# Performance work log

Measured on AMD Instinct MI355X. Metric: run time of the kernel, lower is better.

Reference implementation:

```python
import jax, jax.numpy as jnp
import numpy as np

B, N, P, K, E = 4, 20000, 128, 128, 160000


def setup_inputs() -> dict:
    key = jax.random.key(0)
    ks = jax.random.split(key, 16)
    inv_p = 1.0 / np.sqrt(P)
    inv_3p = 1.0 / np.sqrt(3 * P)
    return {
        "x_in": jax.random.normal(ks[0], (B, N, P), jnp.float32),
        "vertex_areas": jax.random.uniform(ks[1], (B, N), jnp.float32, 1e-3, 1.0),
        "evals": jax.random.uniform(ks[2], (B, K), jnp.float32, 0.0, 10.0),
        "evecs": jax.random.normal(ks[3], (B, N, K), jnp.float32),
        "gradX_vals": jax.random.normal(ks[4], (B, E), jnp.float32),
        "gradY_vals": jax.random.normal(ks[5], (B, E), jnp.float32),
        "grad_rows": jax.random.randint(ks[6], (B, E), 0, N, jnp.int32),
        "grad_cols": jax.random.randint(ks[7], (B, E), 0, N, jnp.int32),
        # learned params
        "diffusion_times": jax.random.uniform(ks[8], (P,), jnp.float32, 1e-3, 0.1),
        "B_re": jax.random.normal(ks[9], (P, P), jnp.float32) * inv_p,
        "B_im": jax.random.normal(ks[10], (P, P), jnp.float32) * inv_p,
        "W1": jax.random.normal(ks[11], (P, 3 * P), jnp.float32) * inv_3p,
        "b1": jnp.zeros((P,), jnp.float32),
        "W2": jax.random.normal(ks[12], (P, P), jnp.float32) * inv_p,
        "b2": jnp.zeros((P,), jnp.float32),
        "W3": jax.random.normal(ks[13], (P, P), jnp.float32) * inv_p,
        "b3": jnp.zeros((P,), jnp.float32),
    }


def _spmm(rows, cols, vals, x):
    # sparse (n,n) @ dense (n,p) via COO gather/scatter
    return jax.ops.segment_sum(vals[:, None] * x[cols], rows, num_segments=x.shape[0])


def reference(x_in, vertex_areas, evals, evecs, gradX_vals, gradY_vals,
              grad_rows, grad_cols, diffusion_times, B_re, B_im,
              W1, b1, W2, b2, W3, b3):
    # SpectralDiffusion: project -> spectral heat scaling -> unproject
    times = jnp.clip(diffusion_times, 1e-8)                       # (P,)
    x_spec = jnp.einsum('bnk,bnp->bkp', evecs, x_in * vertex_areas[..., None])
    scale = jnp.exp(-evals[..., None] * times[None, None, :])     # (B,K,P)
    x_diffuse = jnp.einsum('bnk,bkp->bnp', evecs, scale * x_spec)  # (B,N,P)

    # sparse gradient halves
    gx = jax.vmap(_spmm)(grad_rows, grad_cols, gradX_vals, x_diffuse)  # (B,N,P)
    gy = jax.vmap(_spmm)(grad_rows, grad_cols, gradY_vals, x_diffuse)

    # SpatialGradient: tanh(re*B_re(re) + im*B_im(im))
    x_grad_features = jnp.tanh(gx * (gx @ B_re.T) + gy * (gy @ B_im.T))

    # MiniMLP on concatenated features (dropout inactive in eval)
    h = jnp.concatenate([x_in, x_diffuse, x_grad_features], axis=-1)  # (B,N,3P)
    h = jax.nn.relu(h @ W1.T + b1)
    h = jax.nn.relu(h @ W2.T + b2)
    h = h @ W3.T + b3
    return h + x_in
```

## Files before the change

kernel.cpp:

```cpp
#include <hip/hip_runtime.h>
#include <hip/hip_bf16.h>
#include <cstddef>

#define B_ 4
#define N_ 20000
#define P_ 128
#define K_ 128
#define E_ 160000

constexpr int NCH_S = 79;
constexpr int NSCB  = 79;

typedef __attribute__((ext_vector_type(8))) short short8;
typedef __attribute__((ext_vector_type(4))) float f32x4;

__device__ __forceinline__ unsigned pk2(float x, float y) {
  __hip_bfloat162 h = __float22bfloat162_rn(make_float2(x, y));
  union { __hip_bfloat162 h; unsigned u; } c; c.h = h; return c.u;
}
__device__ __forceinline__ float bf2f(short s) {
  union { unsigned u; float f; } c; c.u = ((unsigned)(unsigned short)s) << 16; return c.f;
}
__device__ __forceinline__ short f2bs(float x) {
  union { __hip_bfloat16 h; short s; } c; c.h = __float2bfloat16(x); return c.s;
}

__global__ __launch_bounds__(256)
void k_prep(const float* __restrict__ ev, const float* __restrict__ xin,
            const float* __restrict__ areas,
            __hip_bfloat16* __restrict__ evT, __hip_bfloat16* __restrict__ xT)
{
  const int tn = blockIdx.x, half = blockIdx.y & 1, mat = blockIdx.y >> 1;
  const int b = blockIdx.z, t = threadIdx.x;
  const int n0 = tn * 64, c0 = half * 64;
  __shared__ float ld[64][65];
  const float* src = (mat ? xin : ev) + (size_t)b * N_ * 128;
  const float* ab  = areas + (size_t)b * N_;
#pragma unroll
  for (int i = 0; i < 4; ++i) {
    int gid = t + i * 256;
    int r = gid >> 4, c4 = (gid & 15) << 2;
    int n = n0 + r;
    float4 v = make_float4(0.f, 0.f, 0.f, 0.f);
    if (n < N_) {
      v = *(const float4*)(src + (size_t)n * 128 + c0 + c4);
      if (mat == 0) { float ar = ab[n]; v.x *= ar; v.y *= ar; v.z *= ar; v.w *= ar; }
    }
    ld[r][c4] = v.x; ld[r][c4+1] = v.y; ld[r][c4+2] = v.z; ld[r][c4+3] = v.w;
  }
  __syncthreads();
  __hip_bfloat16* dst = (mat ? xT : evT) + (size_t)b * 128 * N_;
#pragma unroll
  for (int i = 0; i < 4; ++i) {
    int gid = t + i * 256;
    int cr = gid >> 4, nq = (gid & 15) << 2;
    int n = n0 + nq;
    if (n + 4 <= N_) {
      uint2 u;
      u.x = pk2(ld[nq][cr],   ld[nq+1][cr]);
      u.y = pk2(ld[nq+2][cr], ld[nq+3][cr]);
      *(uint2*)(dst + (size_t)(c0 + cr) * N_ + n) = u;
    }
  }
}

__global__ __launch_bounds__(256)
void k_wprep(const float* __restrict__ Bre, const float* __restrict__ Bim,
             uint4* __restrict__ WfRe, uint4* __restrict__ WfIm)
{
  int fid = blockIdx.x * 256 + threadIdx.x;
  if (fid >= 2048) return;
  int gg = fid >> 7, rr = fid & 127;
  const float* s0 = Bre + rr * 128 + gg * 8;
  const float* s1 = Bim + rr * 128 + gg * 8;
  float4 a0 = *(const float4*)s0, a1 = *(const float4*)(s0 + 4);
  uint4 u; u.x = pk2(a0.x, a0.y); u.y = pk2(a0.z, a0.w);
  u.z = pk2(a1.x, a1.y); u.w = pk2(a1.z, a1.w);
  WfRe[fid] = u;
  float4 b0 = *(const float4*)s1, b1 = *(const float4*)(s1 + 4);
  uint4 v; v.x = pk2(b0.x, b0.y); v.y = pk2(b0.z, b0.w);
  v.z = pk2(b1.x, b1.y); v.w = pk2(b1.z, b1.w);
  WfIm[fid] = v;
}

__global__ __launch_bounds__(256)
void k_wprep_mlp(const float* __restrict__ W1, const float* __restrict__ W2,
                 const float* __restrict__ W3, uint4* __restrict__ W1f,
                 uint4* __restrict__ W2f, uint4* __restrict__ W3f)
{
  int fid = blockIdx.x * 256 + threadIdx.x;
  if (fid >= 10240) return;
  int j = fid >> 11, wi = fid & 2047;
  int gg = wi >> 7, rr = wi & 127;
  const float* src;
  uint4* dst;
  if (j < 3)      { src = W1 + rr * 384 + j * 128 + gg * 8; dst = W1f + j * 2048 + wi; }
  else if (j == 3){ src = W2 + rr * 128 + gg * 8;           dst = W2f + wi; }
  else            { src = W3 + rr * 128 + gg * 8;           dst = W3f + wi; }
  float4 a0 = *(const float4*)src, a1 = *(const float4*)(src + 4);
  uint4 u; u.x = pk2(a0.x, a0.y); u.y = pk2(a0.z, a0.w);
  u.z = pk2(a1.x, a1.y); u.w = pk2(a1.z, a1.w);
  *dst = u;
}

__global__ __launch_bounds__(256)
void k_wprep_spec(const float* __restrict__ sspecT, uint4* __restrict__ sTf)
{
  int fid = blockIdx.x * 256 + threadIdx.x;
  if (fid >= 8192) return;
  int b = fid >> 11, wi = fid & 2047;
  int gg = wi >> 7, p = wi & 127;
  const float* src = sspecT + ((size_t)b * P_ + p) * K_ + gg * 8;
  float4 a0 = *(const float4*)src, a1 = *(const float4*)(src + 4);
  uint4 u; u.x = pk2(a0.x, a0.y); u.y = pk2(a0.z, a0.w);
  u.z = pk2(a1.x, a1.y); u.w = pk2(a1.z, a1.w);
  sTf[(size_t)b * 2048 + wi] = u;
}

__device__ __forceinline__ void stg64(uint4* __restrict__ Ls,
                                      const __hip_bfloat16* __restrict__ G,
                                      int n0, int t)
{
#pragma unroll
  for (int i = 0; i < 2; ++i) {
    int gid = t + i * 512;
    int r = gid >> 3, kg = gid & 7;
    int n = n0 + kg * 8;
    uint4 u = make_uint4(0u, 0u, 0u, 0u);
    if (n < N_) u = *(const uint4*)(G + (size_t)r * N_ + n);
    Ls[r * 8 + (kg ^ (r & 7))] = u;
  }
}

__global__ __launch_bounds__(512)
void k_spec_mm(const __hip_bfloat16* __restrict__ evT,
               const __hip_bfloat16* __restrict__ xT,
               float* __restrict__ part)
{
  const int c = blockIdx.x, b = blockIdx.y, t = threadIdx.x;
  const int l = t & 63, wid = t >> 6;
  const int wr = wid >> 2, wc = wid & 3;
  const int lr = l & 15, lg = l >> 4;
  __shared__ uint4 AsB[1024];
  __shared__ uint4 WsB[1024];
  f32x4 acc[4][2];
#pragma unroll
  for (int m = 0; m < 4; ++m)
#pragma unroll
    for (int n = 0; n < 2; ++n) acc[m][n] = (f32x4)0.f;

  const __hip_bfloat16* eb = evT + (size_t)b * 128 * N_;
  const __hip_bfloat16* xb = xT  + (size_t)b * 128 * N_;

  for (int s = 0; s < 4; ++s) {
    int n0 = c * 256 + s * 64;
    __syncthreads();
    stg64(AsB, eb, n0, t);
    stg64(WsB, xb, n0, t);
    __syncthreads();
    const short8* Ap = (const short8*)AsB;
    const short8* Wp = (const short8*)WsB;
#pragma unroll
    for (int kk = 0; kk < 2; ++kk) {
      int gg = kk * 4 + lg;
      short8 a[4], w[2];
#pragma unroll
      for (int m = 0; m < 4; ++m) { int rr = wr*64 + m*16 + lr; a[m] = Ap[rr*8 + (gg ^ (rr & 7))]; }
#pragma unroll
      for (int n = 0; n < 2; ++n) { int rr = wc*32 + n*16 + lr; w[n] = Wp[rr*8 + (gg ^ (rr & 7))]; }
#pragma unroll
      for (int m = 0; m < 4; ++m)
#pragma unroll
        for (int n = 0; n < 2; ++n)
          acc[m][n] = __builtin_amdgcn_mfma_f32_16x16x32_bf16(a[m], w[n], acc[m][n], 0, 0, 0);
    }
  }

  float* po = part + ((size_t)(b * NCH_S + c) << 14);
#pragma unroll
  for (int m = 0; m < 4; ++m)
#pragma unroll
    for (int r = 0; r < 4; ++r) {
      int row = wr*64 + m*16 + lg*4 + r;
#pragma unroll
      for (int n = 0; n < 2; ++n) {
        int col = wc*32 + n*16 + lr;
        po[row * 128 + col] = acc[m][n][r];
      }
    }
}

__global__ __launch_bounds__(256)
void k_spec_reduce(const float* __restrict__ partial, const float* __restrict__ evals,
                   const float* __restrict__ times, float* __restrict__ sspecT)
{
  int idx = blockIdx.x * 256 + threadIdx.x;
  int b = idx >> 14;
  int kp = idx & 16383;
  int k = kp >> 7, p = kp & 127;
  float s = 0.f;
  const float* pb = partial + (size_t)b * NCH_S * (K_*P_) + kp;
  for (int c = 0; c < NCH_S; ++c) s += pb[(size_t)c * (K_*P_)];
  float tt = times[p]; tt = tt < 1e-8f ? 1e-8f : tt;
  float sc = __expf(-evals[b*K_ + k] * tt);
  sspecT[((size_t)b*P_ + p) * K_ + k] = s * sc;
}

__device__ __forceinline__ void stg64r(uint4* __restrict__ Ls,
                                       const __hip_bfloat16* __restrict__ G,
                                       int nrows, int t)
{
#pragma unroll
  for (int i = 0; i < 4; ++i) {
    int gid = t + i * 256;
    int r = gid >> 4, kg = gid & 15;
    uint4 u = make_uint4(0u,0u,0u,0u);
    if (r < nrows) u = *(const uint4*)(G + (size_t)r * 128 + kg * 8);
    Ls[r * 16 + (kg ^ (r & 7))] = u;
  }
}

__device__ __forceinline__ void stg64r_f32(uint4* __restrict__ Ls,
                                           const float* __restrict__ G,
                                           int nrows, int t)
{
#pragma unroll
  for (int i = 0; i < 4; ++i) {
    int gid = t + i * 256;
    int r = gid >> 4, kg = gid & 15;
    float4 v0 = make_float4(0.f,0.f,0.f,0.f), v1 = v0;
    if (r < nrows) {
      const float* p = G + (size_t)r * 128 + kg * 8;
      v0 = *(const float4*)p;
      v1 = *(const float4*)(p + 4);
    }
    uint4 u;
    u.x = pk2(v0.x, v0.y); u.y = pk2(v0.z, v0.w);
    u.z = pk2(v1.x, v1.y); u.w = pk2(v1.z, v1.w);
    Ls[r * 16 + (kg ^ (r & 7))] = u;
  }
}

__device__ __forceinline__ void mfma_pass64(const uint4* As, const uint4* __restrict__ Wf,
                                            int wc, int lr, int lg, f32x4 acc[4][2])
{
  const short8* Ap = (const short8*)As;
  const short8* Wp = (const short8*)Wf;
#pragma unroll
  for (int kk = 0; kk < 4; ++kk) {
    int gg = kk * 4 + lg;
    short8 a[4], w[2];
#pragma unroll
    for (int m = 0; m < 4; ++m) { int rr = m*16 + lr; a[m] = Ap[rr*16 + (gg ^ (rr & 7))]; }
#pragma unroll
    for (int n = 0; n < 2; ++n) { int rr = wc*32 + n*16 + lr; w[n] = Wp[(gg << 7) + rr]; }
#pragma unroll
    for (int m = 0; m < 4; ++m)
#pragma unroll
      for (int n = 0; n < 2; ++n)
        acc[m][n] = __builtin_amdgcn_mfma_f32_16x16x32_bf16(a[m], w[n], acc[m][n], 0, 0, 0);
  }
}

__global__ __launch_bounds__(256)
void k_unproj(const float* __restrict__ evecs, const uint4* __restrict__ sTf,
              __hip_bfloat16* __restrict__ xd)
{
  const int b = blockIdx.y, r0 = blockIdx.x * 64, t = threadIdx.x;
  const int l = t & 63, w = t >> 6;
  const int lr = l & 15, lg = l >> 4;
  __shared__ uint4 LA[1024];
  f32x4 acc[4][2];
#pragma unroll
  for (int m = 0; m < 4; ++m)
#pragma unroll
    for (int n = 0; n < 2; ++n) acc[m][n] = (f32x4)0.f;
  const int nrows = min(64, N_ - r0);
  stg64r_f32(LA, evecs + (size_t)b * N_ * 128 + (size_t)r0 * 128, nrows, t);
  __syncthreads();
  mfma_pass64(LA, sTf + (size_t)b * 2048, w, lr, lg, acc);
  __hip_bfloat16* xdb = xd + (size_t)b * N_ * P_;
#pragma unroll
  for (int m = 0; m < 4; ++m)
#pragma unroll
    for (int r = 0; r < 4; ++r) {
      int row = r0 + m*16 + lg*4 + r;
      if (row >= N_) continue;
#pragma unroll
      for (int n = 0; n < 2; ++n) {
        int col = w*32 + n*16 + lr;
        xdb[(size_t)row*128 + col] = __float2bfloat16(acc[m][n][r]);
      }
    }
}

__global__ __launch_bounds__(256)
void k_grad(const uint4* __restrict__ WfRe, const uint4* __restrict__ WfIm,
            __hip_bfloat16* __restrict__ gx, const __hip_bfloat16* __restrict__ gy)
{
  const int b = blockIdx.y, r0 = blockIdx.x * 64, t = threadIdx.x;
  const int l = t & 63, wc = t >> 6;
  const int lr = l & 15, lg = l >> 4;
  __shared__ uint4 As[1024];
  __shared__ uint4 As2[1024];
  f32x4 acc1[4][2], acc2[4][2];
#pragma unroll
  for (int m = 0; m < 4; ++m)
#pragma unroll
    for (int n = 0; n < 2; ++n) { acc1[m][n] = (f32x4)0.f; acc2[m][n] = (f32x4)0.f; }

  __hip_bfloat16*       gxb = gx + (size_t)b * N_ * P_;
  const __hip_bfloat16* gyb = gy + (size_t)b * N_ * P_;
  const int nrows = min(64, N_ - r0);

  stg64r(As,  gxb + (size_t)r0 * 128, nrows, t);
  stg64r(As2, gyb + (size_t)r0 * 128, nrows, t);
  __syncthreads();
  mfma_pass64(As,  WfRe, wc, lr, lg, acc1);
  mfma_pass64(As2, WfIm, wc, lr, lg, acc2);
  __syncthreads();

  short* S1 = (short*)As;
  short* S2 = (short*)As2;
#pragma unroll
  for (int m = 0; m < 4; ++m)
#pragma unroll
    for (int r = 0; r < 4; ++r) {
      int rowt = m*16 + lg*4 + r;
#pragma unroll
      for (int n = 0; n < 2; ++n) {
        int col = wc*32 + n*16 + lr;
        int idx = (rowt*16 + ((col>>3) ^ (rowt & 7)))*8 + (col & 7);
        S1[idx] = f2bs(acc1[m][n][r]);
        S2[idx] = f2bs(acc2[m][n][r]);
      }
    }
  __syncthreads();

  {
    const int row = t >> 2, cq = t & 3;
    if (row < nrows) {
      const short8* P1 = (const short8*)As;
      const short8* P2 = (const short8*)As2;
      const size_t gbase = (size_t)(r0 + row) * 128 + cq * 32;
#pragma unroll
      for (int cg = 0; cg < 4; ++cg) {
        int kg = cq * 4 + cg;
        short8 a1 = P1[row*16 + (kg ^ (row & 7))];
        short8 a2 = P2[row*16 + (kg ^ (row & 7))];
        uint4 ux = *(const uint4*)(gxb + gbase + cg*8);
        uint4 uy = *(const uint4*)(gyb + gbase + cg*8);
        unsigned xw[4] = {ux.x, ux.y, ux.z, ux.w};
        unsigned yw[4] = {uy.x, uy.y, uy.z, uy.w};
        unsigned ow[4];
#pragma unroll
        for (int p = 0; p < 4; ++p) {
          float g1l = __uint_as_float(xw[p] << 16);
          float g1h = __uint_as_float(xw[p] & 0xffff0000u);
          float g2l = __uint_as_float(yw[p] << 16);
          float g2h = __uint_as_float(yw[p] & 0xffff0000u);
          float sl = g1l * bf2f(a1[2*p])   + g2l * bf2f(a2[2*p]);
          float sh = g1h * bf2f(a1[2*p+1]) + g2h * bf2f(a2[2*p+1]);
          sl = fminf(fmaxf(sl, -15.f), 15.f);
          sh = fminf(fmaxf(sh, -15.f), 15.f);
          float el = __expf(2.f * sl), eh = __expf(2.f * sh);
          ow[p] = pk2((el - 1.f) / (el + 1.f), (eh - 1.f) / (eh + 1.f));
        }
        uint4 o; o.x = ow[0]; o.y = ow[1]; o.z = ow[2]; o.w = ow[3];
        *(uint4*)(gxb + gbase + cg*8) = o;
      }
    }
  }
}

__global__ __launch_bounds__(256)
void k_mlp(const float* __restrict__ xin, const __hip_bfloat16* __restrict__ xd,
           const __hip_bfloat16* __restrict__ xg,
           const uint4* __restrict__ W1f, const uint4* __restrict__ W2f,
           const uint4* __restrict__ W3f,
           const float* __restrict__ b1, const float* __restrict__ b2,
           const float* __restrict__ b3, float* __restrict__ out)
{
  const int b = blockIdx.y, r0 = blockIdx.x * 64, t = threadIdx.x;
  const int l = t & 63, w = t >> 6;
  const int lr = l & 15, lg = l >> 4;
  __shared__ uint4 LA[1024];
  __shared__ uint4 LB[1024];
  const int nrows = min(64, N_ - r0);
  const float* xinb = xin + (size_t)b * N_ * 128 + (size_t)r0 * 128;

  f32x4 acc[4][2];
#pragma unroll
  for (int m = 0; m < 4; ++m)
#pragma unroll
    for (int n = 0; n < 2; ++n) acc[m][n] = (f32x4)0.f;

  for (int kc = 0; kc < 3; ++kc) {
    __syncthreads();
    if (kc == 0)      stg64r_f32(LA, xinb, nrows, t);
    else if (kc == 1) stg64r(LA, xd + (size_t)b * N_ * 128 + (size_t)r0 * 128, nrows, t);
    else              stg64r(LA, xg + (size_t)b * N_ * 128 + (size_t)r0 * 128, nrows, t);
    __syncthreads();
    mfma_pass64(LA, W1f + kc * 2048, w, lr, lg, acc);
  }
  {
    float bb[2] = { b1[w*32 + lr], b1[w*32 + 16 + lr] };
    short* Sh = (short*)LB;
#pragma unroll
    for (int m = 0; m < 4; ++m)
#pragma unroll
      for (int r = 0; r < 4; ++r) {
        int rowt = m*16 + lg*4 + r;
#pragma unroll
        for (int n = 0; n < 2; ++n) {
          int col = w*32 + n*16 + lr;
          float v = fmaxf(acc[m][n][r] + bb[n], 0.f);
          Sh[(rowt*16 + ((col>>3) ^ (rowt & 7)))*8 + (col & 7)] = f2bs(v);
        }
      }
  }
  __syncthreads();

#pragma unroll
  for (int m = 0; m < 4; ++m)
#pragma unroll
    for (int n = 0; n < 2; ++n) acc[m][n] = (f32x4)0.f;
  mfma_pass64(LB, W2f, w, lr, lg, acc);
  __syncthreads();
  {
    float bb[2] = { b2[w*32 + lr], b2[w*32 + 16 + lr] };
    short* Sh = (short*)LB;
#pragma unroll
    for (int m = 0; m < 4; ++m)
#pragma unroll
      for (int r = 0; r < 4; ++r) {
        int rowt = m*16 + lg*4 + r;
#pragma unroll
        for (int n = 0; n < 2; ++n) {
          int col = w*32 + n*16 + lr;
          float v = fmaxf(acc[m][n][r] + bb[n], 0.f);
          Sh[(rowt*16 + ((col>>3) ^ (rowt & 7)))*8 + (col & 7)] = f2bs(v);
        }
      }
  }
  __syncthreads();

#pragma unroll
  for (int m = 0; m < 4; ++m)
#pragma unroll
    for (int n = 0; n < 2; ++n) acc[m][n] = (f32x4)0.f;
  mfma_pass64(LB, W3f, w, lr, lg, acc);
  __syncthreads();

  {
    float bb[2] = { b3[w*32 + lr], b3[w*32 + 16 + lr] };
    float* F1 = (float*)LA;
    float* F2 = (float*)LB;
#pragma unroll
    for (int m = 0; m < 4; ++m)
#pragma unroll
      for (int r = 0; r < 4; ++r) {
        int rowt = m*16 + lg*4 + r;
#pragma unroll
        for (int n = 0; n < 2; ++n) {
          int col = w*32 + n*16 + lr;
          float v = acc[m][n][r] + bb[n];
          if (col < 64) F1[rowt*64 + col] = v;
          else          F2[rowt*64 + col - 64] = v;
        }
      }
  }
  __syncthreads();

  {
    const int row = t >> 2, cq = t & 3;
    if (row < nrows) {
      const float* Fs = (cq < 2) ? (const float*)LA : (const float*)LB;
      const float* fbase = Fs + row*64 + (cq & 1)*32;
      const float* xr = xinb + (size_t)row * 128 + cq * 32;
      float* orow = out + (size_t)b * N_ * 128 + (size_t)(r0 + row) * 128 + cq * 32;
#pragma unroll
      for (int j = 0; j < 8; ++j) {
        float4 s = ((const float4*)fbase)[j];
        float4 xv = ((const float4*)xr)[j];
        float4 o; o.x = s.x + xv.x; o.y = s.y + xv.y;
        o.z = s.z + xv.z; o.w = s.w + xv.w;
        ((float4*)orow)[j] = o;
      }
    }
  }
}

__global__ void k_count(const int* __restrict__ rows, int* __restrict__ cnt)
{
  int b = blockIdx.y;
  int e = blockIdx.x * 256 + threadIdx.x;
  if (e < E_) atomicAdd(&cnt[b*N_ + rows[(size_t)b*E_ + e]], 1);
}

__global__ __launch_bounds__(256)
void k_scan_blk(const int* __restrict__ cnt, int* __restrict__ off,
                int* __restrict__ bsum)
{
  const int c = blockIdx.x, b = blockIdx.y, t = threadIdx.x;
  const int lane = t & 63, wid = t >> 6;
  __shared__ int wt[4];
  int i = c * 256 + t;
  int v = (i < N_) ? cnt[b*N_ + i] : 0;
  int x = v;
#pragma unroll
  for (int ofs = 1; ofs < 64; ofs <<= 1) {
    int y = __shfl_up(x, ofs, 64);
    if (lane >= ofs) x += y;
  }
  if (lane == 63) wt[wid] = x;
  __syncthreads();
  int wofs = 0;
  for (int wj = 0; wj < wid; ++wj) wofs += wt[wj];
  if (i < N_) off[b*(N_+1) + i] = wofs + x - v;
  if (t == 255) bsum[b*128 + c] = wofs + x;
}

__global__ __launch_bounds__(64)
void k_scan_top(int* __restrict__ bsum, int* __restrict__ off)
{
  const int b = blockIdx.x, t = threadIdx.x;
  int running = 0;
  for (int base = 0; base < 128; base += 64) {
    int i = base + t;
    int v = (i < NSCB) ? bsum[b*128 + i] : 0;
    int x = v;
#pragma unroll
    for (int ofs = 1; ofs < 64; ofs <<= 1) {
      int y = __shfl_up(x, ofs, 64);
      if (t >= ofs) x += y;
    }
    if (i < 128) bsum[b*128 + i] = running + x - v;
    running += __shfl(x, 63, 64);
  }
  if (t == 0) off[b*(N_+1) + N_] = running;
}

__global__ __launch_bounds__(256)
void k_scan_add(const int* __restrict__ bsum, int* __restrict__ off,
                int* __restrict__ pos)
{
  const int c = blockIdx.x, b = blockIdx.y;
  int i = c * 256 + (int)threadIdx.x;
  if (i < N_) {
    int o = off[b*(N_+1) + i] + bsum[b*128 + c];
    off[b*(N_+1) + i] = o;
    pos[b*N_ + i] = o;
  }
}

__global__ void k_fill(const int* __restrict__ rows, const int* __restrict__ cols,
                       const float* __restrict__ vx, const float* __restrict__ vy,
                       int* __restrict__ pos, uint4* __restrict__ prec)
{
  int b = blockIdx.y;
  int e = blockIdx.x * 256 + threadIdx.x;
  if (e < E_) {
    size_t be = (size_t)b*E_ + e;
    int r = rows[be];
    int p = atomicAdd(&pos[b*N_ + r], 1);
    if (p >= 0 && p < E_) {
      uint4 rec;
      rec.x = (unsigned)cols[be];
      rec.y = __float_as_uint(vx[be]);
      rec.z = __float_as_uint(vy[be]);
      rec.w = 0u;
      prec[(size_t)b*E_ + p] = rec;
    }
  }
}

__global__ __launch_bounds__(256)
void k_gather(const __hip_bfloat16* __restrict__ xd, const uint4* __restrict__ prec,
              const int* __restrict__ off,
              __hip_bfloat16* __restrict__ gx, __hip_bfloat16* __restrict__ gy)
{
  const int b = blockIdx.y;
  const int row = (blockIdx.x * 256 + threadIdx.x) >> 6;
  const int lane = threadIdx.x & 63;
  const int q = lane >> 4, ql = lane & 15;
  if (row >= N_) return;
  const int s = off[b*(N_+1) + row], e = off[b*(N_+1) + row + 1];
  float ax[8], ay[8];
#pragma unroll
  for (int k = 0; k < 8; ++k) { ax[k] = 0.f; ay[k] = 0.f; }
  const __hip_bfloat16* xdb = xd + (size_t)b * N_ * P_;
  const uint4* pb = prec + (size_t)b * E_;

  for (int i = s; i < e; i += 8) {
    int idx0 = i + q, idx1 = i + 4 + q;
    bool v0 = idx0 < e, v1 = idx1 < e;
    uint4 rec0 = pb[v0 ? idx0 : (e - 1)];
    uint4 rec1 = pb[v1 ? idx1 : (e - 1)];
    float fx0 = v0 ? __uint_as_float(rec0.y) : 0.f;
    float fy0 = v0 ? __uint_as_float(rec0.z) : 0.f;
    float fx1 = v1 ? __uint_as_float(rec1.y) : 0.f;
    float fy1 = v1 ? __uint_as_float(rec1.z) : 0.f;
    uint4 va = *(const uint4*)(xdb + (size_t)rec0.x * P_ + ql * 8);
    uint4 vb = *(const uint4*)(xdb + (size_t)rec1.x * P_ + ql * 8);
    unsigned aw[4] = {va.x, va.y, va.z, va.w};
    unsigned bw[4] = {vb.x, vb.y, vb.z, vb.w};
#pragma unroll
    for (int p = 0; p < 4; ++p) {
      float a_lo = __uint_as_float(aw[p] << 16);
      float a_hi = __uint_as_float(aw[p] & 0xffff0000u);
      float b_lo = __uint_as_float(bw[p] << 16);
      float b_hi = __uint_as_float(bw[p] & 0xffff0000u);
      ax[2*p]   = fmaf(fx0, a_lo, ax[2*p]);   ax[2*p]   = fmaf(fx1, b_lo, ax[2*p]);
      ax[2*p+1] = fmaf(fx0, a_hi, ax[2*p+1]); ax[2*p+1] = fmaf(fx1, b_hi, ax[2*p+1]);
      ay[2*p]   = fmaf(fy0, a_lo, ay[2*p]);   ay[2*p]   = fmaf(fy1, b_lo, ay[2*p]);
      ay[2*p+1] = fmaf(fy0, a_hi, ay[2*p+1]); ay[2*p+1] = fmaf(fy1, b_hi, ay[2*p+1]);
    }
  }
#pragma unroll
  for (int k = 0; k < 8; ++k) {
    ax[k] += __shfl_xor(ax[k], 16, 64); ax[k] += __shfl_xor(ax[k], 32, 64);
    ay[k] += __shfl_xor(ay[k], 16, 64); ay[k] += __shfl_xor(ay[k], 32, 64);
  }
  if (lane < 16) {
    size_t o = (size_t)b * N_ * P_ + (size_t)row * P_ + ql * 8;
    uint4 ux, uy;
    ux.x = pk2(ax[0], ax[1]); ux.y = pk2(ax[2], ax[3]);
    ux.z = pk2(ax[4], ax[5]); ux.w = pk2(ax[6], ax[7]);
    uy.x = pk2(ay[0], ay[1]); uy.y = pk2(ay[2], ay[3]);
    uy.z = pk2(ay[4], ay[5]); uy.w = pk2(ay[6], ay[7]);
    *(uint4*)(gx + o) = ux;
    *(uint4*)(gy + o) = uy;
  }
}

extern "C" void kernel_launch(void* const* d_in, const int* in_sizes, int n_in,
                              void* d_out, int out_size, void* d_ws, size_t ws_size,
                              hipStream_t stream)
{
  const float* x_in  = (const float*)d_in[0];
  const float* areas = (const float*)d_in[1];
  const float* evals = (const float*)d_in[2];
  const float* evecs = (const float*)d_in[3];
  const float* gXv   = (const float*)d_in[4];
  const float* gYv   = (const float*)d_in[5];
  const int*   grows = (const int*)d_in[6];
  const int*   gcols = (const int*)d_in[7];
  const float* times = (const float*)d_in[8];
  const float* Bre   = (const float*)d_in[9];
  const float* Bim   = (const float*)d_in[10];
  const float* W1    = (const float*)d_in[11];
  const float* b1    = (const float*)d_in[12];
  const float* W2    = (const float*)d_in[13];
  const float* b2    = (const float*)d_in[14];
  const float* W3    = (const float*)d_in[15];
  const float* b3    = (const float*)d_in[16];

  float* ws = (float*)d_ws;
  __hip_bfloat16* xd_bf = (__hip_bfloat16*)ws;
  float*          part  = ws + 6000000;
  __hip_bfloat16* gx_bf = (__hip_bfloat16*)(ws + 12000000);
  __hip_bfloat16* gy_bf = (__hip_bfloat16*)(ws + 18000000);
  __hip_bfloat16* evT   = gx_bf;
  __hip_bfloat16* xT    = gy_bf;

  uint4* prec   = (uint4*)(ws + 24000000);
  int*   ipos   = (int*)(ws + 26560000);
  int*   ioff   = ipos + B_*N_;
  float* sspecT = ws + 26750000;
  uint4* WfRe   = (uint4*)(ws + 26816000);
  uint4* WfIm   = WfRe + 2048;
  int*   bsum   = (int*)(WfIm + 2048);
  uint4* W1f    = (uint4*)(ws + 26834000);
  uint4* W2f    = W1f + 6144;
  uint4* W3f    = W2f + 2048;
  uint4* sTf    = W3f + 2048;
  float* out    = (float*)d_out;

  const int TN = (N_ + 63) / 64;

  k_prep<<<dim3(TN, 4, B_), 256, 0, stream>>>(evecs, x_in, areas, evT, xT);
  k_wprep<<<dim3(8), 256, 0, stream>>>(Bre, Bim, WfRe, WfIm);
  k_wprep_mlp<<<dim3(40), 256, 0, stream>>>(W1, W2, W3, W1f, W2f, W3f);
  k_spec_mm<<<dim3(NCH_S, B_), 512, 0, stream>>>(evT, xT, part);
  k_spec_reduce<<<dim3(B_*K_*P_/256), 256, 0, stream>>>(part, evals, times, sspecT);
  k_wprep_spec<<<dim3(32), 256, 0, stream>>>(sspecT, sTf);
  k_unproj<<<dim3(TN, B_), 256, 0, stream>>>(evecs, sTf, xd_bf);
  hipMemsetAsync(ipos, 0, (size_t)B_*N_*sizeof(int), stream);
  k_count<<<dim3(E_/256, B_), 256, 0, stream>>>(grows, ipos);
  k_scan_blk<<<dim3(NSCB, B_), 256, 0, stream>>>(ipos, ioff, bsum);
  k_scan_top<<<dim3(B_), 64, 0, stream>>>(bsum, ioff);
  k_scan_add<<<dim3(NSCB, B_), 256, 0, stream>>>(bsum, ioff, ipos);
  k_fill<<<dim3(E_/256, B_), 256, 0, stream>>>(grows, gcols, gXv, gYv, ipos, prec);
  k_gather<<<dim3(N_/4, B_), 256, 0, stream>>>(xd_bf, prec, ioff, gx_bf, gy_bf);
  k_grad<<<dim3(TN, B_), 256, 0, stream>>>(WfRe, WfIm, gx_bf, gy_bf);
  k_mlp<<<dim3(TN, B_), 256, 0, stream>>>(x_in, xd_bf, gx_bf, W1f, W2f, W3f,
                                          b1, b2, b3, out);
}
```

Measured before the change: 238.5 us.

## Stage all three MLP input chunks up front and write output directly from accumulators

The MLP kernel now loads x_in, x_diffuse and the gradient features into three separate LDS buffers with a single barrier, instead of a load/sync/compute loop run three times. The epilogue drops its LDS round-trip: each thread adds the bias and the x_in residual and writes the output straight from the MFMA accumulators. This removes several barriers and LDS traffic and lets the global loads overlap. In exchange LDS use goes from 32KB to 64KB per block, which can lower occupancy, and the output stores become scalar and less coalesced.

```diff
diff --git a/kernel.cpp b/kernel.cpp
--- a/kernel.cpp
+++ b/kernel.cpp
@@ -384,25 +384,27 @@
   const int b = blockIdx.y, r0 = blockIdx.x * 64, t = threadIdx.x;
   const int l = t & 63, w = t >> 6;
   const int lr = l & 15, lg = l >> 4;
-  __shared__ uint4 LA[1024];
+  __shared__ uint4 LA0[1024];
+  __shared__ uint4 LA1[1024];
+  __shared__ uint4 LA2[1024];
   __shared__ uint4 LB[1024];
   const int nrows = min(64, N_ - r0);
   const float* xinb = xin + (size_t)b * N_ * 128 + (size_t)r0 * 128;
 
+  stg64r_f32(LA0, xinb, nrows, t);
+  stg64r(LA1, xd + (size_t)b * N_ * 128 + (size_t)r0 * 128, nrows, t);
+  stg64r(LA2, xg + (size_t)b * N_ * 128 + (size_t)r0 * 128, nrows, t);
+  __syncthreads();
+
   f32x4 acc[4][2];
 #pragma unroll
   for (int m = 0; m < 4; ++m)
 #pragma unroll
     for (int n = 0; n < 2; ++n) acc[m][n] = (f32x4)0.f;
-
-  for (int kc = 0; kc < 3; ++kc) {
-    __syncthreads();
-    if (kc == 0)      stg64r_f32(LA, xinb, nrows, t);
-    else if (kc == 1) stg64r(LA, xd + (size_t)b * N_ * 128 + (size_t)r0 * 128, nrows, t);
-    else              stg64r(LA, xg + (size_t)b * N_ * 128 + (size_t)r0 * 128, nrows, t);
-    __syncthreads();
-    mfma_pass64(LA, W1f + kc * 2048, w, lr, lg, acc);
-  }
+  mfma_pass64(LA0, W1f,        w, lr, lg, acc);
+  mfma_pass64(LA1, W1f + 2048, w, lr, lg, acc);
+  mfma_pass64(LA2, W1f + 4096, w, lr, lg, acc);
+
   {
     float bb[2] = { b1[w*32 + lr], b1[w*32 + 16 + lr] };
     short* Sh = (short*)LB;
@@ -450,44 +452,22 @@
 #pragma unroll
     for (int n = 0; n < 2; ++n) acc[m][n] = (f32x4)0.f;
   mfma_pass64(LB, W3f, w, lr, lg, acc);
-  __syncthreads();
-
   {
     float bb[2] = { b3[w*32 + lr], b3[w*32 + 16 + lr] };
-    float* F1 = (float*)LA;
-    float* F2 = (float*)LB;
+    float* ob = out + (size_t)b * N_ * 128;
 #pragma unroll
     for (int m = 0; m < 4; ++m)
 #pragma unroll
       for (int r = 0; r < 4; ++r) {
-        int rowt = m*16 + lg*4 + r;
+        int row = r0 + m*16 + lg*4 + r;
+        if (row >= N_) continue;
 #pragma unroll
         for (int n = 0; n < 2; ++n) {
           int col = w*32 + n*16 + lr;
-          float v = acc[m][n][r] + bb[n];
-          if (col < 64) F1[rowt*64 + col] = v;
-          else          F2[rowt*64 + col - 64] = v;
+          float v = acc[m][n][r] + bb[n] + xinb[(size_t)(m*16 + lg*4 + r)*128 + col];
+          ob[(size_t)row*128 + col] = v;
         }
       }
-  }
-  __syncthreads();
-
-  {
-    const int row = t >> 2, cq = t & 3;
-    if (row < nrows) {
-      const float* Fs = (cq < 2) ? (const float*)LA : (const float*)LB;
-      const float* fbase = Fs + row*64 + (cq & 1)*32;
-      const float* xr = xinb + (size_t)row * 128 + cq * 32;
-      float* orow = out + (size_t)b * N_ * 128 + (size_t)(r0 + row) * 128 + cq * 32;
-#pragma unroll
-      for (int j = 0; j < 8; ++j) {
-        float4 s = ((const float4*)fbase)[j];
-        float4 xv = ((const float4*)xr)[j];
-        float4 o; o.x = s.x + xv.x; o.y = s.y + xv.y;
-        o.z = s.z + xv.z; o.w = s.w + xv.w;
-        ((float4*)orow)[j] = o;
-      }
-    }
   }
 }
 
```

New measurement: 246.9 us. 1.04x slower.
